# Performance work log

Hardware: AMD Instinct MI355X
Metric: run time of the kernel (lower is better)

Reference implementation:

```python
import jax, jax.numpy as jnp
import numpy as np

LAMBDA_S = 1.0   # options['lambda_s']
NITER = 100      # options['iter_ihs']

_HS_FILTER = jnp.array([[1/12, 1/6, 1/12],
                        [1/6,  0.0, 1/6 ],
                        [1/12, 1/6, 1/12]], dtype=jnp.float32)


def _smooth(f):
    # f: [n, h, w] -> 3x3 Horn-Schunck weighted average, zero padding (== torch conv2d padding=1)
    k = _HS_FILTER.reshape(1, 1, 3, 3)  # [out_c, in_c, kh, kw]
    return jax.lax.conv_general_dilated(f[:, None], k, window_strides=(1, 1), padding='SAME')[:, 0]


def setup_inputs() -> dict:
    key = jax.random.key(0)
    k1, k2 = jax.random.split(key)
    n, h, w = 8, 256, 256
    x = jax.random.normal(k1, (n, 3, h, w), dtype=jnp.float32)            # [I_t, I_x, I_y]
    old_estimate = jax.random.normal(k2, (n, 2, h, w), dtype=jnp.float32)  # warm-start (u, v)
    return {"x": x, "old_estimate": old_estimate}


def reference(x, old_estimate):
    # x: [n,3,h,w]; old_estimate: [n,2,h,w]
    I_t, I_x, I_y = x[:, 0], x[:, 1], x[:, 2]
    denom = LAMBDA_S ** 2 + I_x ** 2 + I_y ** 2  # iteration-invariant
    u0, v0 = old_estimate[:, 0], old_estimate[:, 1]  # warm_ihs=True

    def step(carry, _):
        u, v = carry
        u_bar = _smooth(u)
        v_bar = _smooth(v)
        der = (I_x * u_bar + I_y * v_bar + I_t) / denom
        return (u_bar - I_x * der, v_bar - I_y * der), None

    (u, v), _ = jax.lax.scan(step, (u0, v0), None, length=NITER)
    return jnp.stack((u, v), axis=1)  # [n,2,h,w]
```

## Files before the change

kernel.cpp:

```cpp
#include <hip/hip_runtime.h>

typedef unsigned long long ull;
typedef float f32x2 __attribute__((ext_vector_type(2)));
#define FMA2(a,b,c) __builtin_elementwise_fma((a),(b),(c))

#define HH 256
#define WW 256
#define PLANE (HH*WW)
#define TILE_R 32
#define TILE_C 64
#define TT 8
#define ER (TILE_R + 2*TT)
#define EC (TILE_C + 2*TT)
#define NCP (EC/2)
#define NRG 16
#define RPT (ER/NRG)
#define NTHR 1024
#define STRIDE 164
#define LSZ (4 + ER*STRIDE + 4)
#define HROW (NCP*4)
#define HBUFSZ (2*NRG*2*HROW)

#define RING_OFS (2u*1024u*1024u)
#define FLAG_OFS (4u*1024u*1024u)
#define RIMG (HH*(WW/2)*4)
#define NBLK 256

__device__ __forceinline__ float dpp_prev(float v) {
    return __int_as_float(__builtin_amdgcn_update_dpp(0, __float_as_int(v), 0x138, 0xF, 0xF, true));
}
__device__ __forceinline__ float dpp_next(float v) {
    return __int_as_float(__builtin_amdgcn_update_dpp(0, __float_as_int(v), 0x130, 0xF, 0xF, true));
}

__device__ __forceinline__ void hsum2(const float4 M, f32x2& S0, f32x2& S1) {
    f32x2 lo = { M.x, M.y }, hi = { M.z, M.w };
    f32x2 DL = { dpp_prev(M.z), dpp_prev(M.w) };
    f32x2 DR = { dpp_next(M.x), dpp_next(M.y) };
    const f32x2 two = 2.0f;
    S0 = FMA2(two, lo, DL) + hi;
    S1 = FMA2(two, hi, lo) + DR;
}

__device__ __forceinline__ void do_step(
    int q, int S, float* __restrict__ sraw, float* __restrict__ hbuf,
    bool act, int rg, int cp, int r0, int fb,
    float4* __restrict__ Mreg,
    const f32x2 (* __restrict__ CA)[2], const f32x2 (* __restrict__ CB)[2],
    const f32x2 (* __restrict__ CC)[2])
{
    const int par = (q - 1) & 1;
    const bool on = act && (r0 + RPT - 1 >= q - 1) && (r0 <= 48 - q);
    f32x2 S0[RPT+2], S1[RPT+2];

    if (on) {
        #pragma unroll
        for (int j = 0; j < RPT; ++j) hsum2(Mreg[j], S0[j+1], S1[j+1]);
        float* hb = hbuf + (par*NRG + rg)*2*HROW + 4*cp;
        *(float4*)(hb)        = make_float4(S0[1].x,   S0[1].y,   S1[1].x,   S1[1].y);
        *(float4*)(hb + HROW) = make_float4(S0[RPT].x, S0[RPT].y, S1[RPT].x, S1[RPT].y);
    }
    __syncthreads();
    if (on) {
        if (rg > 0) {
            float4 t = *(const float4*)(hbuf + ((par*NRG + rg-1)*2 + 1)*HROW + 4*cp);
            S0[0] = (f32x2){t.x, t.y}; S1[0] = (f32x2){t.z, t.w};
        } else { S0[0] = S0[1]; S1[0] = S1[1]; }
        if (rg < NRG-1) {
            float4 t = *(const float4*)(hbuf + ((par*NRG + rg+1)*2 + 0)*HROW + 4*cp);
            S0[RPT+1] = (f32x2){t.x, t.y}; S1[RPT+1] = (f32x2){t.z, t.w};
        } else { S0[RPT+1] = S0[RPT]; S1[RPT+1] = S1[RPT]; }

        const f32x2 two = 2.0f, m4 = -4.0f;
        const bool fullwb = (q == S);
        #pragma unroll
        for (int j = 0; j < RPT; ++j) {
            float4 Mc = Mreg[j];
            f32x2 Mlo = { Mc.x, Mc.y }, Mhi = { Mc.z, Mc.w };
            f32x2 T0 = FMA2(m4, Mlo, FMA2(two, S0[j+1], S0[j]) + S0[j+2]);
            f32x2 T1 = FMA2(m4, Mhi, FMA2(two, S1[j+1], S1[j]) + S1[j+2]);
            f32x2 rr0 = FMA2(CA[j][0], T0, -FMA2(CB[j][0], T0.yx, CC[j][0]));
            f32x2 rr1 = FMA2(CA[j][1], T1, -FMA2(CB[j][1], T1.yx, CC[j][1]));
            float4 nv = make_float4(rr0.x, rr0.y, rr1.x, rr1.y);
            Mreg[j] = nv;
            if (fullwb) *(float4*)(sraw + STRIDE*(r0 + j) + fb) = nv;
        }
    }
}

__global__ __launch_bounds__(NTHR, 4)
void hs_mega(const float* __restrict__ x,
             const float* __restrict__ est,
             float* __restrict__ out,
             float* __restrict__ ws)
{
    __shared__ __align__(16) float sraw[LSZ];
    __shared__ __align__(16) float hbuf[HBUFSZ];

    const int img = blockIdx.x, cs = blockIdx.y, rb = blockIdx.z;
    const int tid = threadIdx.x;
    const int er0 = rb*TILE_R - TT;
    const int ec0 = cs*TILE_C - TT;
    const int blin = (img*4 + cs)*8 + rb;
    unsigned* flags = (unsigned*)(ws + FLAG_OFS);

    int nb = -1;
    if (tid < 8) {
        int t = (tid < 4) ? tid : tid + 1;
        int dr = t/3 - 1, dc = t%3 - 1;
        int nrb = rb + dr, ncs = cs + dc;
        if (nrb >= 0 && nrb < 8 && ncs >= 0 && ncs < 4)
            nb = (img*4 + ncs)*8 + nrb;
    }

    const int cp = tid & 63;
    const int rg = tid >> 6;
    const bool act = (cp < NCP);
    const int r0 = rg * RPT;
    const int fb = 4 + 4*cp;

    f32x2 CA[RPT][2], CB[RPT][2], CC[RPT][2];
    if (act) {
        const float* __restrict__ xit = x + img*3*PLANE;
        const float* __restrict__ xix = xit + PLANE;
        const float* __restrict__ xiy = xix + PLANE;
        #pragma unroll
        for (int i = 0; i < RPT; ++i) {
            int gr = er0 + r0 + i;
            #pragma unroll
            for (int j = 0; j < 2; ++j) {
                int gc = ec0 + 2*cp + j;
                float A=0.f, B=0.f, C=0.f, D=0.f, E=0.f;
                if (gr >= 0 && gr < HH && gc >= 0 && gc < WW) {
                    int q = gr*WW + gc;
                    float it = xit[q], ix = xix[q], iy = xiy[q];
                    float rd = 1.0f / (1.0f + ix*ix + iy*iy);
                    const float s12 = 1.0f/12.0f;
                    A = (1.0f - ix*ix*rd) * s12;
                    B = (ix*iy*rd) * s12;
                    C = ix*it*rd;
                    D = (1.0f - iy*iy*rd) * s12;
                    E = iy*it*rd;
                }
                CA[i][j] = (f32x2){ A, D };
                CB[i][j] = (f32x2){ B, B };
                CC[i][j] = (f32x2){ C, E };
            }
        }
    }

    {
        const float* __restrict__ eu = est + img*2*PLANE;
        const float* __restrict__ ev = eu + PLANE;
        for (int k = tid; k < ER*NCP; k += NTHR) {
            int r = k / NCP, c = k - r*NCP;
            int gr = er0 + r, gc = ec0 + 2*c;
            float2 uu = make_float2(0.f,0.f), vv = make_float2(0.f,0.f);
            if (gr >= 0 && gr < HH && gc >= 0 && gc < WW) {
                uu = *(const float2*)(eu + gr*WW + gc);
                vv = *(const float2*)(ev + gr*WW + gc);
            }
            *(float4*)(sraw + 4 + STRIDE*r + 4*c) = make_float4(uu.x, vv.x, uu.y, vv.y);
        }
    }
    __syncthreads();

    float4 Mreg[RPT];
    if (act) {
        #pragma unroll
        for (int j = 0; j < RPT; ++j)
            Mreg[j] = *(const float4*)(sraw + STRIDE*(r0 + j) + fb);
    }

    for (int p = 0; p < 13; ++p) {
        if (p < 12) {
            #pragma unroll
            for (int q = 1; q <= 8; ++q)
                do_step(q, 8, sraw, hbuf, act, rg, cp, r0, fb, Mreg, CA, CB, CC);
        } else {
            #pragma unroll
            for (int q = 1; q <= 4; ++q)
                do_step(q, 4, sraw, hbuf, act, rg, cp, r0, fb, Mreg, CA, CB, CC);
        }
        __syncthreads();

        if (p < 12) {
            float* ring = ws + (unsigned)(p & 1) * RING_OFS + img*RIMG;

            for (int k = tid; k < 640; k += NTHR) {
                int m = k; int r, c2;
                if (m < 256)      { r = m >> 5;              c2 = m & 31; }
                else if (m < 512) { r = 24 + ((m-256) >> 5); c2 = (m-256) & 31; }
                else { int mm = m - 512; r = 8 + (mm >> 3); int t = mm & 7; c2 = (t < 4) ? t : 24 + t; }
                const float* sp = sraw + 4 + STRIDE*(r + TT) + 4*(c2 + 4);
                float* gp = ring + ((rb*TILE_R + r)*(WW/2) + cs*(TILE_C/2) + c2)*4;
                __hip_atomic_store((ull*)gp,     *(const ull*)sp,       __ATOMIC_RELAXED, __HIP_MEMORY_SCOPE_AGENT);
                __hip_atomic_store((ull*)gp + 1, *(const ull*)(sp + 2), __ATOMIC_RELAXED, __HIP_MEMORY_SCOPE_AGENT);
            }
            asm volatile("s_waitcnt vmcnt(0)" ::: "memory");
            __syncthreads();
            if (tid == 0)
                __hip_atomic_store(&flags[p*NBLK + blin], 0x5eed0100u + (unsigned)p,
                                   __ATOMIC_RELAXED, __HIP_MEMORY_SCOPE_AGENT);
            asm volatile("" ::: "memory");
            if (tid < 8 && nb >= 0) {
                const unsigned tgt = 0x5eed0100u + (unsigned)p;
                while (__hip_atomic_load(&flags[p*NBLK + nb],
                                         __ATOMIC_RELAXED, __HIP_MEMORY_SCOPE_AGENT) != tgt)
                    __builtin_amdgcn_s_sleep(1);
            }
            __syncthreads();

            for (int k = tid; k < 896; k += NTHR) {
                int m = k; int r, c2;
                if (m < 320)      { r = m / 40;              c2 = m - (m/40)*40; }
                else if (m < 640) { int mm = m-320; r = 40 + mm/40; c2 = mm - (mm/40)*40; }
                else { int mm = m - 640; r = 8 + (mm >> 3); int t = mm & 7; c2 = (t < 4) ? t : 32 + t; }
                int gr = er0 + r, gc2 = cs*(TILE_C/2) - 4 + c2;
                ull v0 = 0, v1 = 0;
                if (gr >= 0 && gr < HH && gc2 >= 0 && gc2 < WW/2) {
                    const float* gp = ring + (gr*(WW/2) + gc2)*4;
                    v0 = __hip_atomic_load((const ull*)gp,     __ATOMIC_RELAXED, __HIP_MEMORY_SCOPE_AGENT);
                    v1 = __hip_atomic_load((const ull*)gp + 1, __ATOMIC_RELAXED, __HIP_MEMORY_SCOPE_AGENT);
                }
                float* sp = sraw + 4 + STRIDE*r + 4*c2;
                *(ull*)sp = v0;
                *(ull*)(sp + 2) = v1;
            }
            __syncthreads();

            if (act) {
                #pragma unroll
                for (int j = 0; j < RPT; ++j) {
                    int r = r0 + j;
                    if (r < TT || r >= ER-TT || cp < 4 || cp >= NCP-4)
                        Mreg[j] = *(const float4*)(sraw + STRIDE*r + fb);
                }
            }
        }
    }

    {
        float* ou = out + img*2*PLANE;
        float* ov = ou + PLANE;
        for (int k = tid; k < 1024; k += NTHR) {
            int r = k >> 5, c2 = k & 31;
            float4 V = *(const float4*)(sraw + 4 + STRIDE*(r + TT) + 4*(c2 + 4));
            int q = (rb*TILE_R + r)*WW + cs*TILE_C + 2*c2;
            *(float2*)(ou + q) = make_float2(V.x, V.z);
            *(float2*)(ov + q) = make_float2(V.y, V.w);
        }
    }
}

extern "C" void kernel_launch(void* const* d_in, const int* in_sizes, int n_in,
                              void* d_out, int out_size, void* d_ws, size_t ws_size,
                              hipStream_t stream) {
    const float* x   = (const float*)d_in[0];
    const float* est = (const float*)d_in[1];
    float* out = (float*)d_out;
    float* ws  = (float*)d_ws;

    dim3 grid(8, WW/TILE_C, HH/TILE_R);
    dim3 blk(NTHR);
    hs_mega<<<grid, blk, 0, stream>>>(x, est, out, ws);
}
```

Baseline: 170.1 us.

## Exchange halos directly from registers, bypassing shared-memory staging

Each thread now writes its tile-border values straight from registers to the global exchange ring, and loads neighbour halo values straight from the ring into registers. This replaces the earlier path that wrote back to shared memory, copied shared to global, then global to shared, then shared to registers. It also drops the LDS write-back at the end of each sub-step, one __syncthreads, and the shared-memory staging in the final output write. The cost is that the global accesses are now scattered per thread rather than cooperatively coalesced, and many threads sit idle during the exchange.

```diff
diff --git a/kernel.cpp b/kernel.cpp
--- a/kernel.cpp
+++ b/kernel.cpp
@@ -43,8 +43,8 @@
 }
 
 __device__ __forceinline__ void do_step(
-    int q, int S, float* __restrict__ sraw, float* __restrict__ hbuf,
-    bool act, int rg, int cp, int r0, int fb,
+    int q, float* __restrict__ hbuf,
+    bool act, int rg, int cp, int r0,
     float4* __restrict__ Mreg,
     const f32x2 (* __restrict__ CA)[2], const f32x2 (* __restrict__ CB)[2],
     const f32x2 (* __restrict__ CC)[2])
@@ -72,7 +72,6 @@
         } else { S0[RPT+1] = S0[RPT]; S1[RPT+1] = S1[RPT]; }
 
         const f32x2 two = 2.0f, m4 = -4.0f;
-        const bool fullwb = (q == S);
         #pragma unroll
         for (int j = 0; j < RPT; ++j) {
             float4 Mc = Mreg[j];
@@ -81,9 +80,7 @@
             f32x2 T1 = FMA2(m4, Mhi, FMA2(two, S1[j+1], S1[j]) + S1[j+2]);
             f32x2 rr0 = FMA2(CA[j][0], T0, -FMA2(CB[j][0], T0.yx, CC[j][0]));
             f32x2 rr1 = FMA2(CA[j][1], T1, -FMA2(CB[j][1], T1.yx, CC[j][1]));
-            float4 nv = make_float4(rr0.x, rr0.y, rr1.x, rr1.y);
-            Mreg[j] = nv;
-            if (fullwb) *(float4*)(sraw + STRIDE*(r0 + j) + fb) = nv;
+            Mreg[j] = make_float4(rr0.x, rr0.y, rr1.x, rr1.y);
         }
     }
 }
@@ -176,26 +173,29 @@
         if (p < 12) {
             #pragma unroll
             for (int q = 1; q <= 8; ++q)
-                do_step(q, 8, sraw, hbuf, act, rg, cp, r0, fb, Mreg, CA, CB, CC);
+                do_step(q, hbuf, act, rg, cp, r0, Mreg, CA, CB, CC);
         } else {
             #pragma unroll
             for (int q = 1; q <= 4; ++q)
-                do_step(q, 4, sraw, hbuf, act, rg, cp, r0, fb, Mreg, CA, CB, CC);
-        }
-        __syncthreads();
+                do_step(q, hbuf, act, rg, cp, r0, Mreg, CA, CB, CC);
+        }
 
         if (p < 12) {
             float* ring = ws + (unsigned)(p & 1) * RING_OFS + img*RIMG;
 
-            for (int k = tid; k < 640; k += NTHR) {
-                int m = k; int r, c2;
-                if (m < 256)      { r = m >> 5;              c2 = m & 31; }
-                else if (m < 512) { r = 24 + ((m-256) >> 5); c2 = (m-256) & 31; }
-                else { int mm = m - 512; r = 8 + (mm >> 3); int t = mm & 7; c2 = (t < 4) ? t : 24 + t; }
-                const float* sp = sraw + 4 + STRIDE*(r + TT) + 4*(c2 + 4);
-                float* gp = ring + ((rb*TILE_R + r)*(WW/2) + cs*(TILE_C/2) + c2)*4;
-                __hip_atomic_store((ull*)gp,     *(const ull*)sp,       __ATOMIC_RELAXED, __HIP_MEMORY_SCOPE_AGENT);
-                __hip_atomic_store((ull*)gp + 1, *(const ull*)(sp + 2), __ATOMIC_RELAXED, __HIP_MEMORY_SCOPE_AGENT);
+            if (act) {
+                #pragma unroll
+                for (int j = 0; j < RPT; ++j) {
+                    int r = r0 + j;
+                    int rr = r - TT, cc = cp - 4;
+                    bool inner = (rr >= 0 && rr < TILE_R && cc >= 0 && cc < TILE_C/2);
+                    if (inner && (rr < 8 || rr >= TILE_R-8 || cc < 4 || cc >= TILE_C/2-4)) {
+                        union { float4 f; ull u[2]; } U; U.f = Mreg[j];
+                        float* gp = ring + ((rb*TILE_R + rr)*(WW/2) + cs*(TILE_C/2) + cc)*4;
+                        __hip_atomic_store((ull*)gp,     U.u[0], __ATOMIC_RELAXED, __HIP_MEMORY_SCOPE_AGENT);
+                        __hip_atomic_store((ull*)gp + 1, U.u[1], __ATOMIC_RELAXED, __HIP_MEMORY_SCOPE_AGENT);
+                    }
+                }
             }
             asm volatile("s_waitcnt vmcnt(0)" ::: "memory");
             __syncthreads();
@@ -211,30 +211,22 @@
             }
             __syncthreads();
 
-            for (int k = tid; k < 896; k += NTHR) {
-                int m = k; int r, c2;
-                if (m < 320)      { r = m / 40;              c2 = m - (m/40)*40; }
-                else if (m < 640) { int mm = m-320; r = 40 + mm/40; c2 = mm - (mm/40)*40; }
-                else { int mm = m - 640; r = 8 + (mm >> 3); int t = mm & 7; c2 = (t < 4) ? t : 32 + t; }
-                int gr = er0 + r, gc2 = cs*(TILE_C/2) - 4 + c2;
-                ull v0 = 0, v1 = 0;
-                if (gr >= 0 && gr < HH && gc2 >= 0 && gc2 < WW/2) {
-                    const float* gp = ring + (gr*(WW/2) + gc2)*4;
-                    v0 = __hip_atomic_load((const ull*)gp,     __ATOMIC_RELAXED, __HIP_MEMORY_SCOPE_AGENT);
-                    v1 = __hip_atomic_load((const ull*)gp + 1, __ATOMIC_RELAXED, __HIP_MEMORY_SCOPE_AGENT);
-                }
-                float* sp = sraw + 4 + STRIDE*r + 4*c2;
-                *(ull*)sp = v0;
-                *(ull*)(sp + 2) = v1;
-            }
-            __syncthreads();
-
             if (act) {
                 #pragma unroll
                 for (int j = 0; j < RPT; ++j) {
                     int r = r0 + j;
-                    if (r < TT || r >= ER-TT || cp < 4 || cp >= NCP-4)
-                        Mreg[j] = *(const float4*)(sraw + STRIDE*r + fb);
+                    if (r < TT || r >= ER-TT || cp < 4 || cp >= NCP-4) {
+                        int gr = er0 + r, gc2 = cs*(TILE_C/2) - 4 + cp;
+                        if (gr >= 0 && gr < HH && gc2 >= 0 && gc2 < WW/2) {
+                            const float* gp = ring + (gr*(WW/2) + gc2)*4;
+                            union { float4 f; ull u[2]; } U;
+                            U.u[0] = __hip_atomic_load((const ull*)gp,     __ATOMIC_RELAXED, __HIP_MEMORY_SCOPE_AGENT);
+                            U.u[1] = __hip_atomic_load((const ull*)gp + 1, __ATOMIC_RELAXED, __HIP_MEMORY_SCOPE_AGENT);
+                            Mreg[j] = U.f;
+                        } else {
+                            Mreg[j] = make_float4(0.f, 0.f, 0.f, 0.f);
+                        }
+                    }
                 }
             }
         }
@@ -243,12 +235,17 @@
     {
         float* ou = out + img*2*PLANE;
         float* ov = ou + PLANE;
-        for (int k = tid; k < 1024; k += NTHR) {
-            int r = k >> 5, c2 = k & 31;
-            float4 V = *(const float4*)(sraw + 4 + STRIDE*(r + TT) + 4*(c2 + 4));
-            int q = (rb*TILE_R + r)*WW + cs*TILE_C + 2*c2;
-            *(float2*)(ou + q) = make_float2(V.x, V.z);
-            *(float2*)(ov + q) = make_float2(V.y, V.w);
+        if (act) {
+            #pragma unroll
+            for (int j = 0; j < RPT; ++j) {
+                int r = r0 + j;
+                int rr = r - TT, cc = cp - 4;
+                if (rr >= 0 && rr < TILE_R && cc >= 0 && cc < TILE_C/2) {
+                    int qq = (rb*TILE_R + rr)*WW + cs*TILE_C + 2*cc;
+                    *(float2*)(ou + qq) = make_float2(Mreg[j].x, Mreg[j].z);
+                    *(float2*)(ov + qq) = make_float2(Mreg[j].y, Mreg[j].w);
+                }
+            }
         }
     }
 }
```

New measurement: 179.0 us. 1.05x slower.
